# Optimization experiments

Hardware: AMD Instinct MI355X
Metric: run time of the kernel (lower is better)

The kernel has to match this reference:

```python
import jax, jax.numpy as jnp
import numpy as np

BINS = 6  # torch.histc(bins=6, min=0, max=256) in rarity()


def _border_mask(h, w, dtype):
    m = jnp.ones((h, w), dtype)
    return m.at[0, :].set(0).at[-1, :].set(0).at[:, 0].set(0).at[:, -1].set(0)


def _norm(x, lo, hi, axes):
    # normalize_tensor: map to [lo,hi]; all-zeros if constant map
    mn = x.min(axes, keepdims=True)
    mx = x.max(axes, keepdims=True)
    d = mx - mn
    ds = jnp.where(d == 0, jnp.ones_like(d), d)
    out = (x - mn) / ds * (hi - lo) + lo
    return jnp.where(d == 0, jnp.zeros_like(out), out)


def _ponder(x, axes):
    # map_ponderation: normalize to [0,1] then scale by (max-mean)^2
    w = (x.max(axes, keepdims=True) - x.mean(axes, keepdims=True)) ** 2
    return _norm(x, 0.0, 1.0, axes) * w


def _rarity_all(ch):
    # Vectorized rarity() over all channels. ch: [C,H,W]
    C, H, W = ch.shape
    ch = ch * _border_mask(H, W, ch.dtype)          # zero 1-px border
    ch = _norm(ch, 0.0, 256.0, (1, 2))              # per-channel -> [0,256]
    # torch.histc over [0,256]: bin = floor(v*bins/256), max value in last bin
    bin_idx = jnp.clip((ch * (BINS / 256.0)).astype(jnp.int32), 0, BINS - 1)
    hist = jax.nn.one_hot(bin_idx, BINS, dtype=ch.dtype).sum((1, 2))  # [C,BINS]
    hist = hist / hist.sum(-1, keepdims=True)
    hist = -jnp.log(hist + 1e-4)
    # lookup: (channel*bins - 1).long().clamp(0, bins-1)  (channel in [0,256], as in source)
    lut_idx = jnp.clip((ch * BINS - 1).astype(jnp.int32), 0, BINS - 1)
    dst = hist[jnp.arange(C)[:, None, None], lut_idx]  # [C,H,W] rarity lookup
    dst = _norm(dst, 0.0, 1.0, (1, 2))
    return _ponder(dst, (1, 2))


def _apply_rarity(x):
    # x: [1,C,H,W] -> [H,W]
    ch = x[0]
    H, W = ch.shape[-2:]
    r = _rarity_all(ch)
    # channel 0: ponderated again, no extra border zeroing (as in source)
    p0 = _ponder(r[0], (0, 1))
    rest = r[1:] * _border_mask(H, W, r.dtype)  # channels 1..C-1: border zeroed
    p = p0 + _ponder(rest, (1, 2)).sum(0)
    return _norm(p, 0.0, 1.0, (0, 1))  # threshold=None -> no thresholding


def _resize240(m):
    # T.Resize((240,240), bilinear) ~ half-pixel linear resize
    return jax.image.resize(m, (240, 240), method='linear')


def _forward(layers):
    # group layers into packs by spatial resolution (static, shapes known)
    packs = {}
    for t in layers:
        packs.setdefault(t.shape[-2:], []).append(t)
    group_maps = []
    for pack in packs.values():
        maps = [_resize240(_apply_rarity(t)) for t in pack]
        fused = maps[0] * 0.0
        for m in maps:  # fuse_itti
            fused = fused + _ponder(m, (0, 1))
        group_maps.append(_norm(fused, 0.0, 256.0, (0, 1)))
    groups = jnp.stack(group_maps, -1)  # [240,240,n_packs]
    return groups.sum(-1), groups


def setup_inputs() -> dict:
    key = jax.random.key(0)
    shapes = ([(1, 64, 224, 224)] * 2 + [(1, 128, 112, 112)] * 2 +
              [(1, 256, 56, 56)] * 3 + [(1, 512, 28, 28)] * 3 +
              [(1, 512, 14, 14)] * 3)
    keys = jax.random.split(key, len(shapes))
    return {f"x{i}": jax.random.uniform(keys[i], s, jnp.float32)
            for i, s in enumerate(shapes)}


def reference(x0, x1, x2, x3, x4, x5, x6, x7, x8, x9, x10, x11, x12):
    return _forward([x0, x1, x2, x3, x4, x5, x6, x7, x8, x9, x10, x11, x12])
```

## Files before the change

kernel.cpp:

```cpp
#include <hip/hip_runtime.h>
#include <math.h>

#define NT 13
#define RHW 57600
#define PIXB 8192

typedef unsigned long long ull;

struct Meta {
  const float* x[NT];
  int C[NT];
  int H[NT];
  float hsc[NT];
  int pixOff[NT + 1];
  int nibOff[NT];
  int mmOff[NT + 1];
  int nchMM[NT];
  int pmOff[NT + 1];
};

__device__ __forceinline__ int segOf(const int* off, int b) {
  int t = 0;
  while (t + 1 < NT && b >= off[t + 1]) t++;
  return t;
}

template <int HH>
__device__ __forceinline__ void mm_body(const float* __restrict__ ch, int pix0, int pix1,
                                        float& mn, float& mx) {
  constexpr int W = HH, H = HH;
  int i40 = pix0 >> 2, i41 = pix1 >> 2;
  const float4* __restrict__ P = reinterpret_cast<const float4*>(ch);
  if constexpr (W % 4 == 0) {
    constexpr int W4 = W / 4;
    for (int i4 = i40 + (int)threadIdx.x; i4 < i41; i4 += 256) {
      float4 v = P[i4];
      int h = i4 / W4;
      int c4 = i4 - h * W4;
      if (h > 0 && h < H - 1) {
        mn = fminf(mn, v.y); mx = fmaxf(mx, v.y);
        mn = fminf(mn, v.z); mx = fmaxf(mx, v.z);
        if (c4 != 0)      { mn = fminf(mn, v.x); mx = fmaxf(mx, v.x); }
        if (c4 != W4 - 1) { mn = fminf(mn, v.w); mx = fmaxf(mx, v.w); }
      }
    }
  } else {
    for (int i4 = i40 + (int)threadIdx.x; i4 < i41; i4 += 256) {
      float4 v = P[i4];
#pragma unroll
      for (int j = 0; j < 4; j++) {
        int idx = i4 * 4 + j;
        int h = idx / W, w = idx - h * W;
        bool ok = h > 0 && h < (H - 1) && w > 0 && w < (W - 1);
        float f = (j == 0) ? v.x : (j == 1) ? v.y : (j == 2) ? v.z : v.w;
        if (ok) { mn = fminf(mn, f); mx = fmaxf(mx, f); }
      }
    }
  }
}

__global__ __launch_bounds__(256) void k_minmax(Meta m, float* cpart) {
  int b = blockIdx.x;
  int t = segOf(m.mmOff, b);
  int local = b - m.mmOff[t];
  int nch = m.nchMM[t];
  int c = local / nch, k = local - c * nch;
  int HW = m.H[t] * m.H[t];
  const float* ch = m.x[t] + (size_t)c * HW;
  int pix0 = k * PIXB, pix1 = min(pix0 + PIXB, HW);
  float mn = INFINITY, mx = -INFINITY;
  switch (m.H[t]) {
    case 224: mm_body<224>(ch, pix0, pix1, mn, mx); break;
    case 112: mm_body<112>(ch, pix0, pix1, mn, mx); break;
    case 56:  mm_body<56>(ch, pix0, pix1, mn, mx); break;
    case 28:  mm_body<28>(ch, pix0, pix1, mn, mx); break;
    default:  mm_body<14>(ch, pix0, pix1, mn, mx); break;
  }
#pragma unroll
  for (int o = 32; o > 0; o >>= 1) {
    mn = fminf(mn, __shfl_down(mn, o));
    mx = fmaxf(mx, __shfl_down(mx, o));
  }
  __shared__ float smn[4], smx[4];
  int wid = threadIdx.x >> 6;
  if ((threadIdx.x & 63) == 0) { smn[wid] = mn; smx[wid] = mx; }
  __syncthreads();
  if (threadIdx.x == 0) {
    for (int i = 1; i < 4; i++) { mn = fminf(mn, smn[i]); mx = fmaxf(mx, smx[i]); }
    cpart[2 * b] = mn; cpart[2 * b + 1] = mx;
  }
}

__device__ __forceinline__ void histElem(float f, float mn, float invd, bool intr, int j,
                                         ull& cbin, ull& clut, unsigned& pack) {
  float vv = (f - mn) * invd * 256.0f;
  float tb = fminf(fmaxf(vv * 0.0234375f, 0.f), 5.f);
  int bin = (int)tb;
  float tl = fminf(fmaxf(vv * 6.0f - 1.0f, 0.f), 5.f);
  int li = (int)tl;
  cbin += (ull)intr << (bin * 10);
  clut += (ull)intr << (li * 10);
  pack |= (unsigned)(intr ? li : 7) << (4 * j);
}

template <int HH>
__device__ __forceinline__ void hist_body(const float* __restrict__ ch,
                                          unsigned short* __restrict__ nb,
                                          int pix0, int pix1, float mn, float invd,
                                          ull& cbin, ull& clut) {
  constexpr int W = HH, H = HH;
  int i40 = pix0 >> 2, i41 = pix1 >> 2;
  const float4* __restrict__ P = reinterpret_cast<const float4*>(ch);
  if constexpr (W % 4 == 0) {
    constexpr int W4 = W / 4;
    for (int i4 = i40 + (int)threadIdx.x; i4 < i41; i4 += 256) {
      int h = i4 / W4;
      if (h == 0 || h == H - 1) { nb[i4] = 0x7777u; continue; }
      float4 v = P[i4];
      int c4 = i4 - h * W4;
      unsigned pack = 0;
      histElem(v.x, mn, invd, c4 != 0, 0, cbin, clut, pack);
      histElem(v.y, mn, invd, true, 1, cbin, clut, pack);
      histElem(v.z, mn, invd, true, 2, cbin, clut, pack);
      histElem(v.w, mn, invd, c4 != W4 - 1, 3, cbin, clut, pack);
      nb[i4] = (unsigned short)pack;
    }
  } else {
    for (int i4 = i40 + (int)threadIdx.x; i4 < i41; i4 += 256) {
      float4 v = P[i4];
      unsigned pack = 0;
#pragma unroll
      for (int j = 0; j < 4; j++) {
        int idx = i4 * 4 + j;
        int h = idx / W, w = idx - h * W;
        bool intr = h > 0 && h < (H - 1) && w > 0 && w < (W - 1);
        float f = (j == 0) ? v.x : (j == 1) ? v.y : (j == 2) ? v.z : v.w;
        histElem(f, mn, invd, intr, j, cbin, clut, pack);
      }
      nb[i4] = (unsigned short)pack;
    }
  }
}

__global__ __launch_bounds__(256) void k_histnib(Meta m, const float* __restrict__ cpart,
                                                 unsigned* __restrict__ hpart,
                                                 unsigned short* __restrict__ nib) {
  int b = blockIdx.x;
  int t = segOf(m.mmOff, b);
  int local = b - m.mmOff[t];
  int nch = m.nchMM[t];
  int c = local / nch, k = local - c * nch;
  int H = m.H[t], HW = H * H;
  const float* ch = m.x[t] + (size_t)c * HW;
  int cb = m.mmOff[t] + c * nch;
  float mn = INFINITY, mx = -INFINITY;
  for (int kk = 0; kk < nch; kk++) {
    mn = fminf(mn, cpart[2 * (cb + kk)]);
    mx = fmaxf(mx, cpart[2 * (cb + kk) + 1]);
  }
  mn = fminf(mn, 0.f);
  mx = fmaxf(mx, 0.f);
  float d = mx - mn;
  float invd = d > 0.f ? 1.0f / d : 0.f;
  unsigned short* nb = nib + m.nibOff[t] + (size_t)c * (HW >> 2);
  int pix0 = k * PIXB, pix1 = min(pix0 + PIXB, HW);
  ull cbin = 0ull, clut = 0ull;
  switch (H) {
    case 224: hist_body<224>(ch, nb, pix0, pix1, mn, invd, cbin, clut); break;
    case 112: hist_body<112>(ch, nb, pix0, pix1, mn, invd, cbin, clut); break;
    case 56:  hist_body<56>(ch, nb, pix0, pix1, mn, invd, cbin, clut); break;
    case 28:  hist_body<28>(ch, nb, pix0, pix1, mn, invd, cbin, clut); break;
    default:  hist_body<14>(ch, nb, pix0, pix1, mn, invd, cbin, clut); break;
  }
  unsigned pk[6];
#pragma unroll
  for (int j = 0; j < 6; j++)
    pk[j] = (unsigned)((cbin >> (10 * j)) & 1023ull) |
            ((unsigned)((clut >> (10 * j)) & 1023ull) << 16);
#pragma unroll
  for (int o = 32; o > 0; o >>= 1) {
#pragma unroll
    for (int j = 0; j < 6; j++) pk[j] += __shfl_down(pk[j], o);
  }
  __shared__ unsigned swh[4][12];
  int wid = threadIdx.x >> 6, lane = threadIdx.x & 63;
  if (lane == 0) {
#pragma unroll
    for (int j = 0; j < 6; j++) { swh[wid][j] = pk[j] & 0xffffu; swh[wid][6 + j] = pk[j] >> 16; }
  }
  __syncthreads();
  if (threadIdx.x < 12)
    hpart[12 * b + threadIdx.x] =
        swh[0][threadIdx.x] + swh[1][threadIdx.x] + swh[2][threadIdx.x] + swh[3][threadIdx.x];
}

__device__ __forceinline__ void buildLut(int c, int H, int HW, int cb, int nch,
                                         const float* __restrict__ cpart,
                                         const unsigned* __restrict__ hpart, float* sLut) {
  float mn = INFINITY, mx = -INFINITY;
  unsigned hh[12];
#pragma unroll
  for (int j = 0; j < 12; j++) hh[j] = 0u;
  for (int k = 0; k < nch; k++) {
    mn = fminf(mn, cpart[2 * (cb + k)]);
    mx = fmaxf(mx, cpart[2 * (cb + k) + 1]);
#pragma unroll
    for (int j = 0; j < 12; j++) hh[j] += hpart[12 * (cb + k) + j];
  }
  mn = fminf(mn, 0.f); mx = fmaxf(mx, 0.f);
  float d = mx - mn;
  float invd = d > 0.f ? 1.0f / d : 0.f;
  float fHW = (float)HW;
  int nbp = 4 * H - 4;
  float vb = (0.f - mn) * invd * 256.0f;
  int bin_b = (int)(vb * 0.0234375f);
  bin_b = bin_b < 0 ? 0 : (bin_b > 5 ? 5 : bin_b);
  float ttb = vb * 6.0f - 1.0f;
  int lib = (int)ttb;
  lib = lib < 0 ? 0 : (lib > 5 ? 5 : lib);
  hh[bin_b] += (unsigned)nbp;
  hh[6 + lib] += (unsigned)nbp;
  float hl[6];
#pragma unroll
  for (int j = 0; j < 6; j++) hl[j] = -logf((float)hh[j] / fHW + 1e-4f);
  float mn2 = INFINITY, mx2 = -INFINITY, sum2 = 0.f;
#pragma unroll
  for (int j = 0; j < 6; j++) {
    unsigned cc = hh[6 + j];
    if (cc) { mn2 = fminf(mn2, hl[j]); mx2 = fmaxf(mx2, hl[j]); sum2 += (float)cc * hl[j]; }
  }
  float d2 = mx2 - mn2;
  float RL[6];
  if (d2 > 0.f) {
    float meanN = (sum2 / fHW - mn2) / d2;
    float w = 1.0f - meanN; w *= w;
#pragma unroll
    for (int j = 0; j < 6; j++) RL[j] = (hl[j] - mn2) / d2 * w;
  } else {
#pragma unroll
    for (int j = 0; j < 6; j++) RL[j] = 0.f;
  }
  float LUT[7];
  if (c == 0) {
    float mnr = INFINITY, mxr = -INFINITY, sumr = 0.f;
#pragma unroll
    for (int j = 0; j < 6; j++) {
      unsigned cc = hh[6 + j];
      if (cc) { mnr = fminf(mnr, RL[j]); mxr = fmaxf(mxr, RL[j]); sumr += (float)cc * RL[j]; }
    }
    float dr = mxr - mnr;
    if (dr > 0.f) {
      float meanr = sumr / fHW;
      float wp = mxr - meanr; wp *= wp;
#pragma unroll
      for (int j = 0; j < 6; j++) LUT[j] = (RL[j] - mnr) / dr * wp;
      LUT[6] = LUT[lib];
    } else {
#pragma unroll
      for (int j = 0; j < 7; j++) LUT[j] = 0.f;
    }
  } else {
    float mnr = 0.f, mxr = 0.f, sumr = 0.f;
#pragma unroll
    for (int j = 0; j < 6; j++) {
      int cc = (int)hh[6 + j] - (j == lib ? nbp : 0);
      if (cc > 0) { mnr = fminf(mnr, RL[j]); mxr = fmaxf(mxr, RL[j]); sumr += (float)cc * RL[j]; }
    }
    float dr = mxr - mnr;
    if (dr > 0.f) {
      float meanr = sumr / fHW;
      float wp = mxr - meanr; wp *= wp;
#pragma unroll
      for (int j = 0; j < 6; j++) LUT[j] = (RL[j] - mnr) / dr * wp;
      LUT[6] = (0.f - mnr) / dr * wp;
    } else {
#pragma unroll
      for (int j = 0; j < 7; j++) LUT[j] = 0.f;
    }
  }
#pragma unroll
  for (int j = 0; j < 6; j++) sLut[c * 8 + j] = LUT[j];
  sLut[c * 8 + 6] = LUT[6];
  sLut[c * 8 + 7] = LUT[6];
}

__global__ __launch_bounds__(256) void k_pmap(Meta m, const float* __restrict__ cpart,
                                              const unsigned* __restrict__ hpart,
                                              const unsigned short* __restrict__ nib,
                                              float* __restrict__ pmaps, float* __restrict__ ppart) {
  __shared__ float sLut[512 * 8];
  __shared__ float sAcc[4][256];
  int b = blockIdx.x;
  int t = segOf(m.pmOff, b);
  int blk = b - m.pmOff[t];
  int C = m.C[t], H = m.H[t], HW = H * H, i4n = HW >> 2;
  int nch = m.nchMM[t];
  int tid = threadIdx.x, wid = tid >> 6, lane = tid & 63;
  for (int c = tid; c < C; c += 256)
    buildLut(c, H, HW, m.mmOff[t] + c * nch, nch, cpart, hpart, sLut);
  __syncthreads();
  int i4 = blk * 64 + lane;
  bool act = i4 < i4n;
  float a0 = 0.f, a1 = 0.f, a2 = 0.f, a3 = 0.f;
  if (act) {
    const unsigned short* nb = nib + m.nibOff[t] + i4;
    int cpw = C >> 2;
    int c0 = wid * cpw, c1 = c0 + cpw;
#pragma unroll 4
    for (int c = c0; c < c1; ++c) {
      unsigned n = nb[(size_t)c * i4n];
      a0 += sLut[c * 8 + (int)(n & 7u)];
      a1 += sLut[c * 8 + (int)((n >> 4) & 7u)];
      a2 += sLut[c * 8 + (int)((n >> 8) & 7u)];
      a3 += sLut[c * 8 + (int)((n >> 12) & 7u)];
    }
  }
  *reinterpret_cast<float4*>(&sAcc[wid][lane * 4]) = make_float4(a0, a1, a2, a3);
  __syncthreads();
  if (wid == 0) {
    float bmn = INFINITY, bmx = -INFINITY;
    if (act) {
      float t0 = 0.f, t1 = 0.f, t2 = 0.f, t3 = 0.f;
#pragma unroll
      for (int w = 0; w < 4; w++) {
        const float* s = &sAcc[w][lane * 4];
        t0 += s[0]; t1 += s[1]; t2 += s[2]; t3 += s[3];
      }
      *reinterpret_cast<float4*>(pmaps + (size_t)m.pixOff[t] + (size_t)i4 * 4) =
          make_float4(t0, t1, t2, t3);
      bmn = fminf(fminf(t0, t1), fminf(t2, t3));
      bmx = fmaxf(fmaxf(t0, t1), fmaxf(t2, t3));
    }
#pragma unroll
    for (int o = 32; o > 0; o >>= 1) {
      bmn = fminf(bmn, __shfl_down(bmn, o));
      bmx = fmaxf(bmx, __shfl_down(bmx, o));
    }
    if (lane == 0) { ppart[2 * b] = bmn; ppart[2 * b + 1] = bmx; }
  }
}

__global__ __launch_bounds__(256) void k_resize(Meta m, const float* pmaps, const float* ppart,
                                                float* mmaps, float* rpart) {
  __shared__ float sMnT, sInvT;
  int t = blockIdx.x / 225;
  int blk = blockIdx.x % 225;
  int wid = threadIdx.x >> 6, lane = threadIdx.x & 63;
  if (wid == 0) {
    int n = m.pmOff[t + 1] - m.pmOff[t];
    const float* pp = ppart + (size_t)m.pmOff[t] * 2;
    float mn = INFINITY, mx = -INFINITY;
    for (int i = lane; i < n; i += 64) { mn = fminf(mn, pp[2 * i]); mx = fmaxf(mx, pp[2 * i + 1]); }
#pragma unroll
    for (int o = 32; o > 0; o >>= 1) {
      mn = fminf(mn, __shfl_down(mn, o));
      mx = fmaxf(mx, __shfl_down(mx, o));
    }
    if (lane == 0) {
      float d = mx - mn;
      sMnT = mn; sInvT = d > 0.f ? 1.0f / d : 0.f;
    }
  }
  __syncthreads();
  int pix = blk * 256 + threadIdx.x;
  int H = m.H[t], W = m.H[t];
  const float* p = pmaps + m.pixOff[t];
  float mn = sMnT, a = sInvT;
  int oy = pix / 240, ox = pix - oy * 240;
  float hs = m.hsc[t];
  float sy = ((float)oy + 0.5f) * hs - 0.5f;
  float sx = ((float)ox + 0.5f) * hs - 0.5f;
  float fy0 = floorf(sy), fx0 = floorf(sx);
  float fy = sy - fy0, fx = sx - fx0;
  int iy0 = (int)fy0, ix0 = (int)fx0;
  int y0 = iy0 < 0 ? 0 : (iy0 > H - 1 ? H - 1 : iy0);
  int y1 = iy0 + 1 < 0 ? 0 : (iy0 + 1 > H - 1 ? H - 1 : iy0 + 1);
  int x0 = ix0 < 0 ? 0 : (ix0 > W - 1 ? W - 1 : ix0);
  int x1 = ix0 + 1 < 0 ? 0 : (ix0 + 1 > W - 1 ? W - 1 : ix0 + 1);
  float v00 = p[y0 * W + x0], v01 = p[y0 * W + x1];
  float v10 = p[y1 * W + x0], v11 = p[y1 * W + x1];
  float r = (1.f - fy) * ((1.f - fx) * v00 + fx * v01) + fy * ((1.f - fx) * v10 + fx * v11);
  float mv = (r - mn) * a;
  mmaps[(size_t)t * RHW + pix] = mv;
  float bmn = mv, bmx = mv, bsm = mv;
#pragma unroll
  for (int o = 32; o > 0; o >>= 1) {
    bmn = fminf(bmn, __shfl_down(bmn, o));
    bmx = fmaxf(bmx, __shfl_down(bmx, o));
    bsm += __shfl_down(bsm, o);
  }
  __shared__ float smn[4], smx[4], ssm[4];
  if ((threadIdx.x & 63) == 0) { smn[wid] = bmn; smx[wid] = bmx; ssm[wid] = bsm; }
  __syncthreads();
  if (threadIdx.x == 0) {
    for (int i = 1; i < 4; i++) { bmn = fminf(bmn, smn[i]); bmx = fmaxf(bmx, smx[i]); bsm += ssm[i]; }
    float* rp = rpart + ((size_t)t * 225 + blk) * 3;
    rp[0] = bmn; rp[1] = bmx; rp[2] = bsm;
  }
}

__global__ __launch_bounds__(256) void k_fuse(const float* mmaps, const float* rpart,
                                              float* fusedm, float* fpart) {
  __shared__ float sMn[3], sD[3], sW[3];
  int g = blockIdx.x / 225;
  int blk = blockIdx.x % 225;
  const int gs[6] = {0, 2, 4, 7, 10, 13};
  int nt = gs[g + 1] - gs[g];
  int wid = threadIdx.x >> 6, lane = threadIdx.x & 63;
  if (wid < nt) {
    int t = gs[g] + wid;
    const float* rp = rpart + (size_t)t * 225 * 3;
    float mn = INFINITY, mx = -INFINITY, sm = 0.f;
    for (int i = lane; i < 225; i += 64) {
      mn = fminf(mn, rp[3 * i]); mx = fmaxf(mx, rp[3 * i + 1]); sm += rp[3 * i + 2];
    }
#pragma unroll
    for (int o = 32; o > 0; o >>= 1) {
      mn = fminf(mn, __shfl_down(mn, o));
      mx = fmaxf(mx, __shfl_down(mx, o));
      sm += __shfl_down(sm, o);
    }
    if (lane == 0) {
      float d = mx - mn;
      if (d > 0.f) {
        float mean = sm * (1.0f / 57600.0f);
        float w = mx - mean; w *= w;
        sMn[wid] = mn; sD[wid] = d; sW[wid] = w;
      } else {
        sMn[wid] = 0.f; sD[wid] = 0.f; sW[wid] = 0.f;
      }
    }
  }
  __syncthreads();
  int pix = blk * 256 + threadIdx.x;
  float acc = 0.f;
  for (int k = 0; k < nt; k++) {
    int t = gs[g] + k;
    if (sD[k] > 0.f) acc += (mmaps[(size_t)t * RHW + pix] - sMn[k]) / sD[k] * sW[k];
  }
  fusedm[(size_t)g * RHW + pix] = acc;
  float bmn = acc, bmx = acc;
#pragma unroll
  for (int o = 32; o > 0; o >>= 1) {
    bmn = fminf(bmn, __shfl_down(bmn, o));
    bmx = fmaxf(bmx, __shfl_down(bmx, o));
  }
  __shared__ float smn[4], smx[4];
  if ((threadIdx.x & 63) == 0) { smn[wid] = bmn; smx[wid] = bmx; }
  __syncthreads();
  if (threadIdx.x == 0) {
    for (int i = 1; i < 4; i++) { bmn = fminf(bmn, smn[i]); bmx = fmaxf(bmx, smx[i]); }
    float* fp = fpart + ((size_t)g * 225 + blk) * 2;
    fp[0] = bmn; fp[1] = bmx;
  }
}

__global__ __launch_bounds__(256) void k_out(const float* fusedm, const float* fpart, float* out) {
  __shared__ float fmn[5], finv[5];
  int wid = threadIdx.x >> 6, lane = threadIdx.x & 63;
  for (int g = wid; g < 5; g += 4) {
    const float* fp = fpart + (size_t)g * 225 * 2;
    float mn = INFINITY, mx = -INFINITY;
    for (int i = lane; i < 225; i += 64) {
      mn = fminf(mn, fp[2 * i]); mx = fmaxf(mx, fp[2 * i + 1]);
    }
#pragma unroll
    for (int o = 32; o > 0; o >>= 1) {
      mn = fminf(mn, __shfl_down(mn, o));
      mx = fmaxf(mx, __shfl_down(mx, o));
    }
    if (lane == 0) {
      float d = mx - mn;
      fmn[g] = mn; finv[g] = d > 0.f ? 256.0f / d : 0.f;
    }
  }
  __syncthreads();
  int pix = blockIdx.x * 256 + threadIdx.x;
  float acc = 0.f;
  float* out2 = out + RHW;
#pragma unroll
  for (int g = 0; g < 5; g++) {
    float v = (fusedm[(size_t)g * RHW + pix] - fmn[g]) * finv[g];
    out2[(size_t)pix * 5 + g] = v;
    acc += v;
  }
  out[pix] = acc;
}

extern "C" void kernel_launch(void* const* d_in, const int* in_sizes, int n_in,
                              void* d_out, int out_size, void* d_ws, size_t ws_size,
                              hipStream_t stream) {
  static const int Cs[NT] = {64, 64, 128, 128, 256, 256, 256, 512, 512, 512, 512, 512, 512};
  static const int Hs[NT] = {224, 224, 112, 112, 56, 56, 56, 28, 28, 28, 14, 14, 14};
  Meta m;
  int po = 0, mmb = 0, pmb = 0, nibTot = 0;
  for (int t = 0; t < NT; t++) {
    m.x[t] = (const float*)d_in[t];
    m.C[t] = Cs[t]; m.H[t] = Hs[t];
    m.hsc[t] = (float)((double)Hs[t] / 240.0);
    int HW = Hs[t] * Hs[t];
    m.pixOff[t] = po; po += HW;
    m.nibOff[t] = nibTot; nibTot += Cs[t] * (HW >> 2);
    m.mmOff[t] = mmb;
    m.nchMM[t] = (HW + PIXB - 1) / PIXB;
    mmb += Cs[t] * m.nchMM[t];
    m.pmOff[t] = pmb; pmb += (HW + 255) / 256;
  }
  m.pixOff[NT] = po; m.mmOff[NT] = mmb; m.pmOff[NT] = pmb;

  size_t off = 0;
  auto a16 = [](size_t x) { return (x + 15) & ~(size_t)15; };
#define WALLOC(var, type, count) type* var = (type*)((char*)d_ws + off); off = a16(off + sizeof(type) * (size_t)(count));
  WALLOC(cpart, float, 2 * mmb)
  WALLOC(hpart, unsigned, 12 * mmb)
  WALLOC(nib, unsigned short, nibTot)
  WALLOC(ppart, float, 2 * pmb)
  WALLOC(rpart, float, NT * 225 * 3)
  WALLOC(fpart, float, 5 * 225 * 2)
  WALLOC(pmaps, float, po)
  WALLOC(mmaps, float, NT * RHW)
  WALLOC(fusedm, float, 5 * RHW)
#undef WALLOC

  hipLaunchKernelGGL(k_minmax, dim3(mmb), dim3(256), 0, stream, m, cpart);
  hipLaunchKernelGGL(k_histnib, dim3(mmb), dim3(256), 0, stream, m, cpart, hpart, nib);
  hipLaunchKernelGGL(k_pmap, dim3(pmb), dim3(256), 0, stream, m, cpart, hpart, nib, pmaps, ppart);
  hipLaunchKernelGGL(k_resize, dim3(NT * 225), dim3(256), 0, stream, m, pmaps, ppart, mmaps, rpart);
  hipLaunchKernelGGL(k_fuse, dim3(5 * 225), dim3(256), 0, stream, mmaps, rpart, fusedm, fpart);
  hipLaunchKernelGGL(k_out, dim3(225), dim3(256), 0, stream, fusedm, fpart, (float*)d_out);
}
```

Measured before the change: 77.25 us.

## Fuse min/max and histogram passes for single-chunk channels into one kernel

Merges the min/max reduction and the histogram/nibble pass into one kernel for channels that fit in one block (resolutions up to 112 after PIXB grows to 12544). The channel is then read a second time while it is likely still in cache, and a full-grid launch is avoided for most channels. Only the 224x224 channels, which still span several blocks, go through a separate histogram kernel launched over just those blocks. In exchange, single-block channels keep the whole channel in one 256-thread block, so those blocks run longer and there is less parallelism.

```diff
diff --git a/kernel.cpp b/kernel.cpp
--- a/kernel.cpp
+++ b/kernel.cpp
@@ -3,7 +3,7 @@
 
 #define NT 13
 #define RHW 57600
-#define PIXB 8192
+#define PIXB 12544
 
 typedef unsigned long long ull;
 
@@ -56,38 +56,6 @@
         if (ok) { mn = fminf(mn, f); mx = fmaxf(mx, f); }
       }
     }
-  }
-}
-
-__global__ __launch_bounds__(256) void k_minmax(Meta m, float* cpart) {
-  int b = blockIdx.x;
-  int t = segOf(m.mmOff, b);
-  int local = b - m.mmOff[t];
-  int nch = m.nchMM[t];
-  int c = local / nch, k = local - c * nch;
-  int HW = m.H[t] * m.H[t];
-  const float* ch = m.x[t] + (size_t)c * HW;
-  int pix0 = k * PIXB, pix1 = min(pix0 + PIXB, HW);
-  float mn = INFINITY, mx = -INFINITY;
-  switch (m.H[t]) {
-    case 224: mm_body<224>(ch, pix0, pix1, mn, mx); break;
-    case 112: mm_body<112>(ch, pix0, pix1, mn, mx); break;
-    case 56:  mm_body<56>(ch, pix0, pix1, mn, mx); break;
-    case 28:  mm_body<28>(ch, pix0, pix1, mn, mx); break;
-    default:  mm_body<14>(ch, pix0, pix1, mn, mx); break;
-  }
-#pragma unroll
-  for (int o = 32; o > 0; o >>= 1) {
-    mn = fminf(mn, __shfl_down(mn, o));
-    mx = fmaxf(mx, __shfl_down(mx, o));
-  }
-  __shared__ float smn[4], smx[4];
-  int wid = threadIdx.x >> 6;
-  if ((threadIdx.x & 63) == 0) { smn[wid] = mn; smx[wid] = mx; }
-  __syncthreads();
-  if (threadIdx.x == 0) {
-    for (int i = 1; i < 4; i++) { mn = fminf(mn, smn[i]); mx = fmaxf(mx, smx[i]); }
-    cpart[2 * b] = mn; cpart[2 * b + 1] = mx;
   }
 }
 
@@ -142,7 +110,78 @@
   }
 }
 
-__global__ __launch_bounds__(256) void k_histnib(Meta m, const float* __restrict__ cpart,
+__global__ __launch_bounds__(256) void k_front(Meta m, float* __restrict__ cpart,
+                                               unsigned* __restrict__ hpart,
+                                               unsigned short* __restrict__ nib) {
+  __shared__ float smn[4], smx[4];
+  __shared__ float sMnS, sInvS;
+  __shared__ unsigned swh[4][12];
+  int b = blockIdx.x;
+  int t = segOf(m.mmOff, b);
+  int local = b - m.mmOff[t];
+  int nch = m.nchMM[t];
+  int c = local / nch, k = local - c * nch;
+  int H = m.H[t], HW = H * H;
+  const float* ch = m.x[t] + (size_t)c * HW;
+  int tid = threadIdx.x, wid = tid >> 6, lane = tid & 63;
+  int pix0 = k * PIXB, pix1 = min(pix0 + PIXB, HW);
+
+  float mn = INFINITY, mx = -INFINITY;
+  switch (H) {
+    case 224: mm_body<224>(ch, pix0, pix1, mn, mx); break;
+    case 112: mm_body<112>(ch, pix0, pix1, mn, mx); break;
+    case 56:  mm_body<56>(ch, pix0, pix1, mn, mx); break;
+    case 28:  mm_body<28>(ch, pix0, pix1, mn, mx); break;
+    default:  mm_body<14>(ch, pix0, pix1, mn, mx); break;
+  }
+#pragma unroll
+  for (int o = 32; o > 0; o >>= 1) {
+    mn = fminf(mn, __shfl_down(mn, o));
+    mx = fmaxf(mx, __shfl_down(mx, o));
+  }
+  if (lane == 0) { smn[wid] = mn; smx[wid] = mx; }
+  __syncthreads();
+  if (tid == 0) {
+    for (int i = 1; i < 4; i++) { mn = fminf(mn, smn[i]); mx = fmaxf(mx, smx[i]); }
+    cpart[2 * b] = mn; cpart[2 * b + 1] = mx;
+    if (nch == 1) {
+      float mnf = fminf(mn, 0.f), mxf = fmaxf(mx, 0.f);
+      float d = mxf - mnf;
+      sMnS = mnf; sInvS = d > 0.f ? 1.0f / d : 0.f;
+    }
+  }
+  if (nch > 1) return;
+  __syncthreads();
+  float mnc = sMnS, invd = sInvS;
+
+  unsigned short* nb = nib + m.nibOff[t] + (size_t)c * (HW >> 2);
+  ull cbin = 0ull, clut = 0ull;
+  switch (H) {
+    case 112: hist_body<112>(ch, nb, 0, HW, mnc, invd, cbin, clut); break;
+    case 56:  hist_body<56>(ch, nb, 0, HW, mnc, invd, cbin, clut); break;
+    case 28:  hist_body<28>(ch, nb, 0, HW, mnc, invd, cbin, clut); break;
+    default:  hist_body<14>(ch, nb, 0, HW, mnc, invd, cbin, clut); break;
+  }
+  unsigned pk[6];
+#pragma unroll
+  for (int j = 0; j < 6; j++)
+    pk[j] = (unsigned)((cbin >> (10 * j)) & 1023ull) |
+            ((unsigned)((clut >> (10 * j)) & 1023ull) << 16);
+#pragma unroll
+  for (int o = 32; o > 0; o >>= 1) {
+#pragma unroll
+    for (int j = 0; j < 6; j++) pk[j] += __shfl_down(pk[j], o);
+  }
+  if (lane == 0) {
+#pragma unroll
+    for (int j = 0; j < 6; j++) { swh[wid][j] = pk[j] & 0xffffu; swh[wid][6 + j] = pk[j] >> 16; }
+  }
+  __syncthreads();
+  if (tid < 12)
+    hpart[12 * b + tid] = swh[0][tid] + swh[1][tid] + swh[2][tid] + swh[3][tid];
+}
+
+__global__ __launch_bounds__(256) void k_histbig(Meta m, const float* __restrict__ cpart,
                                                  unsigned* __restrict__ hpart,
                                                  unsigned short* __restrict__ nib) {
   int b = blockIdx.x;
@@ -165,13 +204,7 @@
   unsigned short* nb = nib + m.nibOff[t] + (size_t)c * (HW >> 2);
   int pix0 = k * PIXB, pix1 = min(pix0 + PIXB, HW);
   ull cbin = 0ull, clut = 0ull;
-  switch (H) {
-    case 224: hist_body<224>(ch, nb, pix0, pix1, mn, invd, cbin, clut); break;
-    case 112: hist_body<112>(ch, nb, pix0, pix1, mn, invd, cbin, clut); break;
-    case 56:  hist_body<56>(ch, nb, pix0, pix1, mn, invd, cbin, clut); break;
-    case 28:  hist_body<28>(ch, nb, pix0, pix1, mn, invd, cbin, clut); break;
-    default:  hist_body<14>(ch, nb, pix0, pix1, mn, invd, cbin, clut); break;
-  }
+  hist_body<224>(ch, nb, pix0, pix1, mn, invd, cbin, clut);
   unsigned pk[6];
 #pragma unroll
   for (int j = 0; j < 6; j++)
@@ -493,7 +526,7 @@
   static const int Cs[NT] = {64, 64, 128, 128, 256, 256, 256, 512, 512, 512, 512, 512, 512};
   static const int Hs[NT] = {224, 224, 112, 112, 56, 56, 56, 28, 28, 28, 14, 14, 14};
   Meta m;
-  int po = 0, mmb = 0, pmb = 0, nibTot = 0;
+  int po = 0, mmb = 0, pmb = 0, nibTot = 0, bigCnt = 0;
   for (int t = 0; t < NT; t++) {
     m.x[t] = (const float*)d_in[t];
     m.C[t] = Cs[t]; m.H[t] = Hs[t];
@@ -504,6 +537,7 @@
     m.mmOff[t] = mmb;
     m.nchMM[t] = (HW + PIXB - 1) / PIXB;
     mmb += Cs[t] * m.nchMM[t];
+    if (m.nchMM[t] > 1) bigCnt += Cs[t] * m.nchMM[t];
     m.pmOff[t] = pmb; pmb += (HW + 255) / 256;
   }
   m.pixOff[NT] = po; m.mmOff[NT] = mmb; m.pmOff[NT] = pmb;
@@ -522,8 +556,8 @@
   WALLOC(fusedm, float, 5 * RHW)
 #undef WALLOC
 
-  hipLaunchKernelGGL(k_minmax, dim3(mmb), dim3(256), 0, stream, m, cpart);
-  hipLaunchKernelGGL(k_histnib, dim3(mmb), dim3(256), 0, stream, m, cpart, hpart, nib);
+  hipLaunchKernelGGL(k_front, dim3(mmb), dim3(256), 0, stream, m, cpart, hpart, nib);
+  hipLaunchKernelGGL(k_histbig, dim3(bigCnt), dim3(256), 0, stream, m, cpart, hpart, nib);
   hipLaunchKernelGGL(k_pmap, dim3(pmb), dim3(256), 0, stream, m, cpart, hpart, nib, pmaps, ppart);
   hipLaunchKernelGGL(k_resize, dim3(NT * 225), dim3(256), 0, stream, m, pmaps, ppart, mmaps, rpart);
   hipLaunchKernelGGL(k_fuse, dim3(5 * 225), dim3(256), 0, stream, mmaps, rpart, fusedm, fpart);
```

New measurement: 76.09 us. About the same (-1.5%).
